# Performance work log

Measured on AMD Instinct MI355X. Metric: run time of the kernel, lower is better.

## Reference

```python
import jax, jax.numpy as jnp
import numpy as np

TEMPERATURE = 0.5


def setup_inputs() -> dict:
    key = jax.random.key(0)
    k1, k2 = jax.random.split(key)
    B, D = 8192, 128
    z_i = jax.random.normal(k1, (B, D), dtype=jnp.float32)
    z_j = jax.random.normal(k2, (B, D), dtype=jnp.float32)
    return {"z_i": z_i, "z_j": z_j}


def reference(z_i, z_j):
    B = z_i.shape[0]
    eps = 1e-12  # matches torch F.normalize default clamp
    zi = z_i / jnp.maximum(jnp.linalg.norm(z_i, axis=1, keepdims=True), eps)
    zj = z_j / jnp.maximum(jnp.linalg.norm(z_j, axis=1, keepdims=True), eps)
    reps = jnp.concatenate([zi, zj], axis=0)  # [2B, D], unit rows
    # cosine similarity of unit vectors == dot product -> single GEMM
    sim = reps @ reps.T  # [2B, 2B]
    n = 2 * B
    diag = jnp.eye(n, dtype=bool)
    sim = jnp.where(diag, -1e9, sim) / TEMPERATURE
    labels = jnp.concatenate([jnp.arange(B) + B, jnp.arange(B)])  # positive pair indices
    logp = jax.nn.log_softmax(sim, axis=1)
    loss = -jnp.mean(jnp.take_along_axis(logp, labels[:, None], axis=1))
    return loss
```

## Files before the change

kernel.cpp:

```cpp
#include <hip/hip_runtime.h>
#include <hip/hip_bf16.h>

#define NB 8192
#define ND 128
#define N2 16384

#define CPB 512
#define CTILE 64
#define NT (CPB / CTILE)
#define TILEB (CTILE * 128)

typedef __attribute__((ext_vector_type(4))) float f32x4;
typedef __attribute__((ext_vector_type(4))) int v4i;
typedef __attribute__((ext_vector_type(8))) int v8i;

static constexpr float SQRT_C_VAL = 1.69864368f;

__global__ __launch_bounds__(256) void nrm_kernel(const float* __restrict__ zi,
                                                  const float* __restrict__ zj,
                                                  unsigned short* __restrict__ reps8_u16,
                                                  float* __restrict__ pos,
                                                  float* __restrict__ ssum) {
    const int gtid = blockIdx.x * 256 + threadIdx.x;
    if (gtid < N2) ssum[gtid] = 0.f;
    const int pair = gtid >> 6;
    const int lane = threadIdx.x & 63;
    const float2 vi = *reinterpret_cast<const float2*>(zi + pair * ND + lane * 2);
    const float2 vj = *reinterpret_cast<const float2*>(zj + pair * ND + lane * 2);
    float ssi = vi.x * vi.x + vi.y * vi.y;
    float ssj = vj.x * vj.x + vj.y * vj.y;
#pragma unroll
    for (int m = 1; m < 64; m <<= 1) {
        ssi += __shfl_xor(ssi, m);
        ssj += __shfl_xor(ssj, m);
    }
    float ni = fmaxf(sqrtf(ssi), 1e-12f);
    float nj = fmaxf(sqrtf(ssj), 1e-12f);
    const float ii = 1.0f / ni, ij = 1.0f / nj;
    const float uix = vi.x * ii, uiy = vi.y * ii;
    const float ujx = vj.x * ij, ujy = vj.y * ij;
    float d = uix * ujx + uiy * ujy;
#pragma unroll
    for (int m = 1; m < 64; m <<= 1) d += __shfl_xor(d, m);
    if (lane == 0) pos[pair] = d;
    const int pki = __builtin_amdgcn_cvt_pk_fp8_f32(uix * SQRT_C_VAL, uiy * SQRT_C_VAL, 0, false);
    const int pkj = __builtin_amdgcn_cvt_pk_fp8_f32(ujx * SQRT_C_VAL, ujy * SQRT_C_VAL, 0, false);
    reps8_u16[pair * 64 + lane] = (unsigned short)(pki & 0xFFFF);
    reps8_u16[(NB + pair) * 64 + lane] = (unsigned short)(pkj & 0xFFFF);
}

__device__ inline void gload_lds16(const void* g, void* l) {
    __builtin_amdgcn_global_load_lds(
        (const __attribute__((address_space(1))) void*)g,
        (__attribute__((address_space(3))) void*)l, 16, 0, 0);
}

__global__ __launch_bounds__(256, 2) void sim_kernel(const char* __restrict__ reps8,
                                                     float* __restrict__ ssum) {
    __shared__ __align__(16) char lds[4][TILEB];
    const int tid = threadIdx.x;
    const int lane = tid & 63;
    const int wid = tid >> 6;
    const int l15 = lane & 15;
    const int l4 = lane >> 4;
    const int rb = blockIdx.x * 256;
    const int cb = blockIdx.y * CPB;
    const int qb = rb + wid * 64;

    v8i qf[4];
#pragma unroll
    for (int g = 0; g < 4; ++g)
        qf[g] = *reinterpret_cast<const v8i*>(
            reps8 + (size_t)(qb + g * 16 + l15) * 128 + l4 * 32);
    __builtin_amdgcn_sched_barrier(0);
    asm volatile("s_waitcnt vmcnt(0)" ::: "memory");
    __builtin_amdgcn_sched_barrier(0);

    f32x4 sacc[4];
#pragma unroll
    for (int g = 0; g < 4; ++g) sacc[g] = {0.f, 0.f, 0.f, 0.f};

    const char* srcq[2];
#pragma unroll
    for (int q = 0; q < 2; ++q) {
        const int s_lin = q * 256 + tid;
        const int m = s_lin >> 4;
        const int sp = s_lin & 15;
        const int s = sp ^ ((m & 3) << 1);
        const int col = 2 * m + (s & 1);
        const int chunk = s >> 1;
        srcq[q] = reps8 + (size_t)(cb + col) * 128 + chunk * 16;
    }
    auto stage = [&](int t) {
        char* dst0 = &lds[t & 3][(wid * 64) * 16];
        char* dst1 = &lds[t & 3][(256 + wid * 64) * 16];
        gload_lds16(srcq[0] + (size_t)t * TILEB, dst0);
        gload_lds16(srcq[1] + (size_t)t * TILEB, dst1);
    };

    const int h = l15 >> 1;
    const int sloA = (4 * l4 + (l15 & 1)) ^ ((h & 3) << 1);
    const int rdlo = h * 256 + sloA * 16;
    const int rdhi = h * 256 + (sloA ^ 2) * 16;

    stage(0);
    stage(1);
    stage(2);

#pragma unroll 1
    for (int t = 0; t < NT; ++t) {
        if (t + 3 <= NT) {
            asm volatile("s_waitcnt vmcnt(4)" ::: "memory");
        } else if (t + 2 == NT) {
            asm volatile("s_waitcnt vmcnt(2)" ::: "memory");
        } else {
            asm volatile("s_waitcnt vmcnt(0)" ::: "memory");
        }
        __builtin_amdgcn_s_barrier();
        if (t + 3 < NT) stage(t + 3);

        const int tc = cb + t * CTILE;
        const bool dg = ((unsigned)(qb - tc) < 64u);
        const char* lbase = lds[t & 3];
#pragma unroll
        for (int cg = 0; cg < 4; ++cg) {
            const v4i lo = *reinterpret_cast<const v4i*>(lbase + rdlo + cg * 2048);
            const v4i hi = *reinterpret_cast<const v4i*>(lbase + rdhi + cg * 2048);
            const v8i kf = __builtin_shufflevector(lo, hi, 0, 1, 2, 3, 4, 5, 6, 7);
            f32x4 acc[4];
            const f32x4 z4 = {0.f, 0.f, 0.f, 0.f};
#pragma unroll
            for (int g = 0; g < 4; ++g)
                acc[g] = __builtin_amdgcn_mfma_scale_f32_16x16x128_f8f6f4(
                    qf[g], kf, z4, 0, 0, 0, 0x7F7F7F7F, 0, 0x7F7F7F7F);
#pragma unroll
            for (int g = 0; g < 4; ++g) {
                f32x4 e;
#pragma unroll
                for (int r = 0; r < 4; ++r) e[r] = __builtin_amdgcn_exp2f(acc[g][r]);
                if (dg) {
                    const int col_abs = tc + cg * 16 + l15;
                    const int row0 = qb + g * 16 + l4 * 4;
#pragma unroll
                    for (int r = 0; r < 4; ++r)
                        if (row0 + r == col_abs) e[r] = 0.f;
                }
                sacc[g] += e;
            }
        }
    }

#pragma unroll
    for (int g = 0; g < 4; ++g) {
#pragma unroll
        for (int r = 0; r < 4; ++r) {
#pragma unroll
            for (int m = 1; m < 16; m <<= 1) sacc[g][r] += __shfl_xor(sacc[g][r], m);
        }
    }
    if (l15 == 0) {
#pragma unroll
        for (int g = 0; g < 4; ++g)
#pragma unroll
            for (int r = 0; r < 4; ++r)
                atomicAdd(&ssum[qb + g * 16 + l4 * 4 + r], sacc[g][r]);
    }
}

__global__ __launch_bounds__(1024) void fin_kernel(const float* __restrict__ ssum,
                                                   const float* __restrict__ pos,
                                                   float* __restrict__ out) {
    const int tid = threadIdx.x;
    float acc = 0.f;
    for (int r = tid; r < N2; r += 1024) {
        const int p = (r < NB) ? r : r - NB;
        acc += logf(ssum[r]) - 2.0f * pos[p];
    }
#pragma unroll
    for (int m = 1; m < 64; m <<= 1) acc += __shfl_xor(acc, m);
    __shared__ float red[16];
    const int wid = tid >> 6, lane = tid & 63;
    if (lane == 0) red[wid] = acc;
    __syncthreads();
    if (wid == 0) {
        float v = (lane < 16) ? red[lane] : 0.f;
#pragma unroll
        for (int m = 1; m < 16; m <<= 1) v += __shfl_xor(v, m);
        if (lane == 0) out[0] = v / (float)N2;
    }
}

extern "C" void kernel_launch(void* const* d_in, const int* in_sizes, int n_in,
                              void* d_out, int out_size, void* d_ws, size_t ws_size,
                              hipStream_t stream) {
    const float* zi = (const float*)d_in[0];
    const float* zj = (const float*)d_in[1];
    float* out = (float*)d_out;
    char* ws = (char*)d_ws;

    char* reps8 = ws;
    float* pos = (float*)(ws + (size_t)N2 * ND);
    float* ssum = pos + NB;

    nrm_kernel<<<NB / 4, 256, 0, stream>>>(zi, zj, (unsigned short*)reps8, pos, ssum);
    dim3 grid(N2 / 256, N2 / CPB);
    sim_kernel<<<grid, 256, 0, stream>>>(reps8, ssum);
    fin_kernel<<<1, 1024, 0, stream>>>(ssum, pos, out);
}
```

Baseline: 58.69 us.

## Subtract self-similarity term in finalize and split sim blocks into eight waves

The diagonal masking is removed from the inner loop of the similarity kernel. The normalize kernel instead computes each row's fp8-quantized self dot product, and the finalize kernel subtracts exp2 of it from the row sum. Separately, each block now runs 512 threads, with each wave handling 32 query rows instead of 64 and issuing one staging load per tile. This cuts per-wave register use, adds occupancy, and removes the diagonal branch and compares. The risks are that the self-term computed in fp32 may not exactly match the MFMA result, causing cancellation error, and that each wave now does fewer MFMAs per LDS read.

```diff
diff --git a/kernel.cpp b/kernel.cpp
--- a/kernel.cpp
+++ b/kernel.cpp
@@ -20,7 +20,8 @@
                                                   const float* __restrict__ zj,
                                                   unsigned short* __restrict__ reps8_u16,
                                                   float* __restrict__ pos,
-                                                  float* __restrict__ ssum) {
+                                                  float* __restrict__ ssum,
+                                                  float* __restrict__ sdiag) {
     const int gtid = blockIdx.x * 256 + threadIdx.x;
     if (gtid < N2) ssum[gtid] = 0.f;
     const int pair = gtid >> 6;
@@ -47,6 +48,21 @@
     const int pkj = __builtin_amdgcn_cvt_pk_fp8_f32(ujx * SQRT_C_VAL, ujy * SQRT_C_VAL, 0, false);
     reps8_u16[pair * 64 + lane] = (unsigned short)(pki & 0xFFFF);
     reps8_u16[(NB + pair) * 64 + lane] = (unsigned short)(pkj & 0xFFFF);
+    const float fi0 = __builtin_amdgcn_cvt_f32_fp8(pki, 0);
+    const float fi1 = __builtin_amdgcn_cvt_f32_fp8(pki, 1);
+    const float fj0 = __builtin_amdgcn_cvt_f32_fp8(pkj, 0);
+    const float fj1 = __builtin_amdgcn_cvt_f32_fp8(pkj, 1);
+    float sqi = fi0 * fi0 + fi1 * fi1;
+    float sqj = fj0 * fj0 + fj1 * fj1;
+#pragma unroll
+    for (int m = 1; m < 64; m <<= 1) {
+        sqi += __shfl_xor(sqi, m);
+        sqj += __shfl_xor(sqj, m);
+    }
+    if (lane == 0) {
+        sdiag[pair] = sqi;
+        sdiag[NB + pair] = sqj;
+    }
 }
 
 __device__ inline void gload_lds16(const void* g, void* l) {
@@ -55,7 +71,7 @@
         (__attribute__((address_space(3))) void*)l, 16, 0, 0);
 }
 
-__global__ __launch_bounds__(256, 2) void sim_kernel(const char* __restrict__ reps8,
+__global__ __launch_bounds__(512, 4) void sim_kernel(const char* __restrict__ reps8,
                                                      float* __restrict__ ssum) {
     __shared__ __align__(16) char lds[4][TILEB];
     const int tid = threadIdx.x;
@@ -65,37 +81,29 @@
     const int l4 = lane >> 4;
     const int rb = blockIdx.x * 256;
     const int cb = blockIdx.y * CPB;
-    const int qb = rb + wid * 64;
-
-    v8i qf[4];
-#pragma unroll
-    for (int g = 0; g < 4; ++g)
+    const int qb = rb + wid * 32;
+
+    v8i qf[2];
+#pragma unroll
+    for (int g = 0; g < 2; ++g)
         qf[g] = *reinterpret_cast<const v8i*>(
             reps8 + (size_t)(qb + g * 16 + l15) * 128 + l4 * 32);
     __builtin_amdgcn_sched_barrier(0);
     asm volatile("s_waitcnt vmcnt(0)" ::: "memory");
     __builtin_amdgcn_sched_barrier(0);
 
-    f32x4 sacc[4];
-#pragma unroll
-    for (int g = 0; g < 4; ++g) sacc[g] = {0.f, 0.f, 0.f, 0.f};
-
-    const char* srcq[2];
-#pragma unroll
-    for (int q = 0; q < 2; ++q) {
-        const int s_lin = q * 256 + tid;
-        const int m = s_lin >> 4;
-        const int sp = s_lin & 15;
-        const int s = sp ^ ((m & 3) << 1);
-        const int col = 2 * m + (s & 1);
-        const int chunk = s >> 1;
-        srcq[q] = reps8 + (size_t)(cb + col) * 128 + chunk * 16;
-    }
+    f32x4 sacc[2];
+#pragma unroll
+    for (int g = 0; g < 2; ++g) sacc[g] = {0.f, 0.f, 0.f, 0.f};
+
+    const int m_s = tid >> 4;
+    const int sp_s = tid & 15;
+    const int s_s = sp_s ^ ((m_s & 3) << 1);
+    const char* srcq = reps8 + (size_t)(cb + 2 * m_s + (s_s & 1)) * 128 + (s_s >> 1) * 16;
+
     auto stage = [&](int t) {
-        char* dst0 = &lds[t & 3][(wid * 64) * 16];
-        char* dst1 = &lds[t & 3][(256 + wid * 64) * 16];
-        gload_lds16(srcq[0] + (size_t)t * TILEB, dst0);
-        gload_lds16(srcq[1] + (size_t)t * TILEB, dst1);
+        char* dst = &lds[t & 3][wid * 1024];
+        gload_lds16(srcq + (size_t)t * TILEB, dst);
     };
 
     const int h = l15 >> 1;
@@ -109,49 +117,36 @@
 
 #pragma unroll 1
     for (int t = 0; t < NT; ++t) {
-        if (t + 3 <= NT) {
-            asm volatile("s_waitcnt vmcnt(4)" ::: "memory");
-        } else if (t + 2 == NT) {
+        if (t <= NT - 3) {
             asm volatile("s_waitcnt vmcnt(2)" ::: "memory");
+        } else if (t == NT - 2) {
+            asm volatile("s_waitcnt vmcnt(1)" ::: "memory");
         } else {
             asm volatile("s_waitcnt vmcnt(0)" ::: "memory");
         }
         __builtin_amdgcn_s_barrier();
         if (t + 3 < NT) stage(t + 3);
 
-        const int tc = cb + t * CTILE;
-        const bool dg = ((unsigned)(qb - tc) < 64u);
         const char* lbase = lds[t & 3];
 #pragma unroll
         for (int cg = 0; cg < 4; ++cg) {
             const v4i lo = *reinterpret_cast<const v4i*>(lbase + rdlo + cg * 2048);
             const v4i hi = *reinterpret_cast<const v4i*>(lbase + rdhi + cg * 2048);
             const v8i kf = __builtin_shufflevector(lo, hi, 0, 1, 2, 3, 4, 5, 6, 7);
-            f32x4 acc[4];
             const f32x4 z4 = {0.f, 0.f, 0.f, 0.f};
 #pragma unroll
-            for (int g = 0; g < 4; ++g)
-                acc[g] = __builtin_amdgcn_mfma_scale_f32_16x16x128_f8f6f4(
+            for (int g = 0; g < 2; ++g) {
+                f32x4 acc = __builtin_amdgcn_mfma_scale_f32_16x16x128_f8f6f4(
                     qf[g], kf, z4, 0, 0, 0, 0x7F7F7F7F, 0, 0x7F7F7F7F);
 #pragma unroll
-            for (int g = 0; g < 4; ++g) {
-                f32x4 e;
-#pragma unroll
-                for (int r = 0; r < 4; ++r) e[r] = __builtin_amdgcn_exp2f(acc[g][r]);
-                if (dg) {
-                    const int col_abs = tc + cg * 16 + l15;
-                    const int row0 = qb + g * 16 + l4 * 4;
-#pragma unroll
-                    for (int r = 0; r < 4; ++r)
-                        if (row0 + r == col_abs) e[r] = 0.f;
-                }
-                sacc[g] += e;
+                for (int r = 0; r < 4; ++r)
+                    sacc[g][r] += __builtin_amdgcn_exp2f(acc[r]);
             }
         }
     }
 
 #pragma unroll
-    for (int g = 0; g < 4; ++g) {
+    for (int g = 0; g < 2; ++g) {
 #pragma unroll
         for (int r = 0; r < 4; ++r) {
 #pragma unroll
@@ -160,7 +155,7 @@
     }
     if (l15 == 0) {
 #pragma unroll
-        for (int g = 0; g < 4; ++g)
+        for (int g = 0; g < 2; ++g)
 #pragma unroll
             for (int r = 0; r < 4; ++r)
                 atomicAdd(&ssum[qb + g * 16 + l4 * 4 + r], sacc[g][r]);
@@ -169,12 +164,13 @@
 
 __global__ __launch_bounds__(1024) void fin_kernel(const float* __restrict__ ssum,
                                                    const float* __restrict__ pos,
+                                                   const float* __restrict__ sdiag,
                                                    float* __restrict__ out) {
     const int tid = threadIdx.x;
     float acc = 0.f;
     for (int r = tid; r < N2; r += 1024) {
         const int p = (r < NB) ? r : r - NB;
-        acc += logf(ssum[r]) - 2.0f * pos[p];
+        acc += logf(ssum[r] - exp2f(sdiag[r])) - 2.0f * pos[p];
     }
 #pragma unroll
     for (int m = 1; m < 64; m <<= 1) acc += __shfl_xor(acc, m);
@@ -201,9 +197,10 @@
     char* reps8 = ws;
     float* pos = (float*)(ws + (size_t)N2 * ND);
     float* ssum = pos + NB;
-
-    nrm_kernel<<<NB / 4, 256, 0, stream>>>(zi, zj, (unsigned short*)reps8, pos, ssum);
+    float* sdiag = ssum + N2;
+
+    nrm_kernel<<<NB / 4, 256, 0, stream>>>(zi, zj, (unsigned short*)reps8, pos, ssum, sdiag);
     dim3 grid(N2 / 256, N2 / CPB);
-    sim_kernel<<<grid, 256, 0, stream>>>(reps8, ssum);
-    fin_kernel<<<1, 1024, 0, stream>>>(ssum, pos, out);
-}
+    sim_kernel<<<grid, 512, 0, stream>>>(reps8, ssum);
+    fin_kernel<<<1, 1024, 0, stream>>>(ssum, pos, sdiag, out);
+}
```

Result: no change. 58.09 us (-1.0%).
